# Optimization experiments

Hardware: AMD Instinct MI355X
Metric: run time of the kernel (lower is better)

Reference implementation:

```python
import jax, jax.numpy as jnp
import numpy as np

EPS = 1e-5

def _round_ste(x):
    # straight-through round (identical value in fwd; STE grad in bwd module)
    return x + jax.lax.stop_gradient(jnp.round(x) - x)

def _quant_weight(w, bits):
    # per-tensor symmetric absmax quantization to `bits` bits (BitNet-style)
    qb = float(2 ** (bits - 1) - 1)
    scale = qb / jnp.maximum(jnp.max(jnp.abs(w)), EPS)
    return _round_ste(jnp.clip(w * scale, -qb, qb)) / scale

def _quant_act(x):
    # per-token 8-bit absmax activation quantization
    qb = 127.0
    scale = qb / jnp.maximum(jnp.max(jnp.abs(x), axis=-1, keepdims=True), EPS)
    return _round_ste(jnp.clip(x * scale, -qb, qb)) / scale

def _layernorm(x, gamma, beta):
    mu = jnp.mean(x, axis=-1, keepdims=True)
    var = jnp.mean(jnp.square(x - mu), axis=-1, keepdims=True)
    return (x - mu) * jax.lax.rsqrt(var + EPS) * gamma + beta

def _qlinear(x, w, b, bits):
    return jnp.einsum('btd,fd->btf', _quant_act(x), _quant_weight(w, bits)) + b

def setup_inputs() -> dict:
    key = jax.random.key(0)
    ks = jax.random.split(key, 4)
    B, T, D, F = 8, 2048, 1024, 4096
    return {
        'x': jax.random.normal(ks[0], (B, T, D), dtype=jnp.float32),
        'mask': jnp.ones((B, T, 1), dtype=jnp.float32),
        'ln_gamma': jnp.ones((D,), dtype=jnp.float32),
        'ln_beta': jnp.zeros((D,), dtype=jnp.float32),
        'w1': jax.random.normal(ks[1], (F, D), dtype=jnp.float32) * (1.0 / np.sqrt(D)),
        'b1': jnp.zeros((F,), dtype=jnp.float32),
        'w2': jax.random.normal(ks[2], (D, F), dtype=jnp.float32) * (1.0 / np.sqrt(F)),
        'b2': jnp.zeros((D,), dtype=jnp.float32),
        'bitwidth': 8,
    }

def reference(x, mask, ln_gamma, ln_beta, w1, b1, w2, b2, bitwidth):
    y = _layernorm(x, ln_gamma, ln_beta)           # [B,T,D]
    y = _qlinear(y, w1, b1, bitwidth)              # [B,T,F]
    y = y * jax.nn.sigmoid(y)                      # swish
    y = _qlinear(y, w2, b2, bitwidth)              # [B,T,D]
    seq_mask = mask[:, :, 0][..., None]            # [B,T,1]
    y = y * seq_mask
    return x + 0.5 * y
```

## Files before the change

kernel.cpp:

```cpp
#include <hip/hip_runtime.h>
#include <hip/hip_bf16.h>
#include <stdint.h>


typedef int v4i __attribute__((ext_vector_type(4)));
typedef int v16i __attribute__((ext_vector_type(16)));

#define BK 128

__device__ __forceinline__ float wave_max64(float v) {
#pragma unroll
  for (int off = 32; off; off >>= 1) v = fmaxf(v, __shfl_xor(v, off, 64));
  return v;
}

__device__ __forceinline__ void load16_to_lds(const int8_t* g, int8_t* l) {
  __builtin_amdgcn_global_load_lds((const __attribute__((address_space(1))) void*)g,
                                   (__attribute__((address_space(3))) void*)l, 16, 0, 0);
}

__global__ __launch_bounds__(256) void absmax_kernel(const float* __restrict__ w, int n4,
                                                     int* __restrict__ slot) {
  float m = 0.f;
  const float4* w4 = (const float4*)w;
  for (int i = blockIdx.x * 256 + threadIdx.x; i < n4; i += gridDim.x * 256) {
    float4 v = w4[i];
    m = fmaxf(fmaxf(fabsf(v.x), fabsf(v.y)), fmaxf(fmaxf(fabsf(v.z), fabsf(v.w)), m));
  }
  m = wave_max64(m);
  __shared__ float sm[4];
  int lane = threadIdx.x & 63, wv = threadIdx.x >> 6;
  if (!lane) sm[wv] = m;
  __syncthreads();
  if (!threadIdx.x) {
    m = fmaxf(fmaxf(sm[0], sm[1]), fmaxf(sm[2], sm[3]));
    atomicMax(slot, __float_as_int(m));
  }
}

__global__ void scales_kernel(const int* __restrict__ wmax, const int* __restrict__ bits,
                              float* __restrict__ scal) {
  float qb = (float)((1 << (bits[0] - 1)) - 1);
  scal[2] = qb / fmaxf(__int_as_float(wmax[0]), 1e-5f);
  scal[3] = qb / fmaxf(__int_as_float(wmax[1]), 1e-5f);
  scal[4] = qb;
}

__global__ __launch_bounds__(256) void wquant_kernel(const float* __restrict__ w,
                                                     const float* __restrict__ scal, int which,
                                                     int8_t* __restrict__ out) {
  float s = scal[2 + which], qb = scal[4];
  int i = blockIdx.x * 256 + threadIdx.x;
  float4 v = ((const float4*)w)[i];
  char4 q;
  q.x = (char)(int)rintf(fminf(fmaxf(v.x * s, -qb), qb));
  q.y = (char)(int)rintf(fminf(fmaxf(v.y * s, -qb), qb));
  q.z = (char)(int)rintf(fminf(fmaxf(v.z * s, -qb), qb));
  q.w = (char)(int)rintf(fminf(fmaxf(v.w * s, -qb), qb));
  ((char4*)out)[i] = q;
}

__global__ __launch_bounds__(256) void ln_quant_kernel(const float* __restrict__ x,
                                                       const float* __restrict__ gamma,
                                                       const float* __restrict__ beta,
                                                       int8_t* __restrict__ xq,
                                                       float* __restrict__ xscale) {
  const int row = blockIdx.x;
  const int tid = threadIdx.x;
  const float4 v = ((const float4*)(x + (size_t)row * 1024))[tid];
  float s = v.x + v.y + v.z + v.w;
  float ss = fmaf(v.x, v.x, fmaf(v.y, v.y, fmaf(v.z, v.z, v.w * v.w)));
#pragma unroll
  for (int off = 32; off; off >>= 1) {
    s += __shfl_xor(s, off, 64);
    ss += __shfl_xor(ss, off, 64);
  }
  __shared__ float sm[8];
  const int lane = tid & 63, wv = tid >> 6;
  if (!lane) { sm[wv] = s; sm[4 + wv] = ss; }
  __syncthreads();
  s = sm[0] + sm[1] + sm[2] + sm[3];
  ss = sm[4] + sm[5] + sm[6] + sm[7];
  const float mu = s * (1.f / 1024.f);
  const float var = ss * (1.f / 1024.f) - mu * mu;
  const float rstd = rsqrtf(var + 1e-5f);
  const float4 g = ((const float4*)gamma)[tid];
  const float4 bb = ((const float4*)beta)[tid];
  float y0 = (v.x - mu) * rstd * g.x + bb.x;
  float y1 = (v.y - mu) * rstd * g.y + bb.y;
  float y2 = (v.z - mu) * rstd * g.z + bb.z;
  float y3 = (v.w - mu) * rstd * g.w + bb.w;
  float am = fmaxf(fmaxf(fabsf(y0), fabsf(y1)), fmaxf(fabsf(y2), fabsf(y3)));
  am = wave_max64(am);
  __syncthreads();
  if (!lane) sm[wv] = am;
  __syncthreads();
  am = fmaxf(fmaxf(sm[0], sm[1]), fmaxf(sm[2], sm[3]));
  const float scale = 127.f / fmaxf(am, 1e-5f);
  char4 q;
  q.x = (char)(int)rintf(fminf(fmaxf(y0 * scale, -127.f), 127.f));
  q.y = (char)(int)rintf(fminf(fmaxf(y1 * scale, -127.f), 127.f));
  q.z = (char)(int)rintf(fminf(fmaxf(y2 * scale, -127.f), 127.f));
  q.w = (char)(int)rintf(fminf(fmaxf(y3 * scale, -127.f), 127.f));
  ((char4*)(xq + (size_t)row * 1024))[tid] = q;
  if (!tid) xscale[row] = scale;
}

__global__ __launch_bounds__(256) void hquant_kernel(const ushort* __restrict__ h,
                                                     int8_t* __restrict__ hq,
                                                     float* __restrict__ hscale) {
  const int row = blockIdx.x;
  const int tid = threadIdx.x;
  const int4* p = (const int4*)(h + (size_t)row * 4096);
  union { int4 i4; ushort u[8]; } ua, ub;
  ua.i4 = p[tid * 2];
  ub.i4 = p[tid * 2 + 1];
  float f[16];
#pragma unroll
  for (int i = 0; i < 8; ++i) f[i] = __uint_as_float((unsigned)ua.u[i] << 16);
#pragma unroll
  for (int i = 0; i < 8; ++i) f[8 + i] = __uint_as_float((unsigned)ub.u[i] << 16);
  float am = 0.f;
#pragma unroll
  for (int i = 0; i < 16; ++i) am = fmaxf(am, fabsf(f[i]));
  am = wave_max64(am);
  __shared__ float sm[4];
  const int lane = tid & 63, wv = tid >> 6;
  if (!lane) sm[wv] = am;
  __syncthreads();
  am = fmaxf(fmaxf(sm[0], sm[1]), fmaxf(sm[2], sm[3]));
  const float scale = 127.f / fmaxf(am, 1e-5f);
  union { int4 i4; char c[16]; } q;
#pragma unroll
  for (int i = 0; i < 16; ++i)
    q.c[i] = (char)(int)rintf(fminf(fmaxf(f[i] * scale, -127.f), 127.f));
  ((int4*)(hq + (size_t)row * 4096))[tid] = q.i4;
  if (!tid) hscale[row] = scale;
}

template <int K, int BMt, int BNt>
__device__ __forceinline__ void gemm_core(const int8_t* __restrict__ A,
                                          const int8_t* __restrict__ B, int8_t* As, int8_t* Bs,
                                          v16i (&acc)[BMt / 64][BNt / 64]) {
  constexpr int AM = BMt / 64, AN = BNt / 64;
  const int tid = threadIdx.x;
  const int lane = tid & 63;
  const int wave = tid >> 6;
  const int wm = (wave & 1) * (BMt / 2);
  const int wn = (wave >> 1) * (BNt / 2);
  const int lrow = lane & 31;
  const int half = lane >> 5;
  const int x7 = lrow & 7;
  const size_t m0 = (size_t)blockIdx.y * BMt;
  const size_t n0 = (size_t)blockIdx.x * BNt;

  const int r = tid >> 3;
  const int cs = ((tid & 7) ^ (r & 7)) << 4;
  const int8_t* ga = A + (m0 + r) * K + cs;
  const int8_t* gb = B + (n0 + r) * K + cs;
  int8_t* la = As + tid * 16;
  int8_t* lb = Bs + tid * 16;

  for (int k0 = 0; k0 < K; k0 += BK) {
    __syncthreads();
#pragma unroll
    for (int t = 0; t < BMt / 32; ++t)
      load16_to_lds(ga + (size_t)(t * 32) * K + k0, la + t * 4096);
#pragma unroll
    for (int t = 0; t < BNt / 32; ++t)
      load16_to_lds(gb + (size_t)(t * 32) * K + k0, lb + t * 4096);
    __syncthreads();
#pragma unroll
    for (int ks = 0; ks < 4; ++ks) {
      const int so = ((ks * 2 + half) ^ x7) << 4;
      v4i af[AM], bf[AN];
#pragma unroll
      for (int i = 0; i < AM; ++i)
        af[i] = *(const v4i*)(As + (wm + i * 32 + lrow) * 128 + so);
#pragma unroll
      for (int j = 0; j < AN; ++j)
        bf[j] = *(const v4i*)(Bs + (wn + j * 32 + lrow) * 128 + so);
#pragma unroll
      for (int i = 0; i < AM; ++i)
#pragma unroll
        for (int j = 0; j < AN; ++j)
          acc[i][j] = __builtin_amdgcn_mfma_i32_32x32x32_i8(af[i], bf[j], acc[i][j], 0, 0, 0);
    }
  }
}

__global__ __launch_bounds__(256, 2) void gemm1_kernel(const int8_t* __restrict__ Aq,
                                                       const int8_t* __restrict__ Bq,
                                                       const float* __restrict__ xscale,
                                                       const float* __restrict__ scal,
                                                       const float* __restrict__ bias,
                                                       ushort* __restrict__ H) {
  __shared__ __align__(16) int8_t As[128 * 128];
  __shared__ __align__(16) int8_t Bs[256 * 128];
  v16i acc[2][4] = {};
  gemm_core<1024, 128, 256>(Aq, Bq, As, Bs, acc);
  const float sw1 = scal[2];
  const int lane = threadIdx.x & 63;
  const int wave = threadIdx.x >> 6;
  const int m0 = blockIdx.y * 128 + (wave & 1) * 64;
  const int n0 = blockIdx.x * 256 + (wave >> 1) * 128;
  const int cn = lane & 31;
  const int h4 = (lane >> 5) << 2;
#pragma unroll
  for (int i = 0; i < 2; ++i) {
#pragma unroll
    for (int reg = 0; reg < 16; ++reg) {
      const int row = (reg & 3) + ((reg >> 2) << 3) + h4;
      const int m = m0 + i * 32 + row;
      const float rcp = 1.0f / (xscale[m] * sw1);
#pragma unroll
      for (int j = 0; j < 4; ++j) {
        const int n = n0 + j * 32 + cn;
        const float v = (float)acc[i][j][reg] * rcp + bias[n];
        const float hsw = v / (1.0f + __expf(-v));
        __hip_bfloat16 hb = __float2bfloat16(hsw);
        H[(size_t)m * 4096 + n] = *(const ushort*)&hb;
      }
    }
  }
}

__global__ __launch_bounds__(256, 2) void gemm2_kernel(const int8_t* __restrict__ Aq,
                                                       const int8_t* __restrict__ Bq,
                                                       const float* __restrict__ hscale,
                                                       const float* __restrict__ scal,
                                                       const float* __restrict__ bias,
                                                       const float* __restrict__ x,
                                                       const float* __restrict__ mask,
                                                       float* __restrict__ out) {
  __shared__ __align__(16) int8_t As[256 * 128];
  __shared__ __align__(16) int8_t Bs[128 * 128];
  v16i acc[4][2] = {};
  gemm_core<4096, 256, 128>(Aq, Bq, As, Bs, acc);
  const float sw2 = scal[3];
  const int lane = threadIdx.x & 63;
  const int wave = threadIdx.x >> 6;
  const int m0 = blockIdx.y * 256 + (wave & 1) * 128;
  const int n0 = blockIdx.x * 128 + (wave >> 1) * 64;
  const int cn = lane & 31;
  const int h4 = (lane >> 5) << 2;
#pragma unroll
  for (int i = 0; i < 4; ++i) {
#pragma unroll
    for (int reg = 0; reg < 16; ++reg) {
      const int row = (reg & 3) + ((reg >> 2) << 3) + h4;
      const int m = m0 + i * 32 + row;
      const float rcp = 1.0f / (hscale[m] * sw2);
      const float mk = 0.5f * mask[m];
#pragma unroll
      for (int j = 0; j < 2; ++j) {
        const int n = n0 + j * 32 + cn;
        const float v = (float)acc[i][j][reg] * rcp + bias[n];
        const size_t idx = (size_t)m * 1024 + n;
        out[idx] = x[idx] + mk * v;
      }
    }
  }
}

extern "C" void kernel_launch(void* const* d_in, const int* in_sizes, int n_in, void* d_out,
                              int out_size, void* d_ws, size_t ws_size, hipStream_t stream) {
  const float* x = (const float*)d_in[0];
  const float* mask = (const float*)d_in[1];
  const float* gamma = (const float*)d_in[2];
  const float* beta = (const float*)d_in[3];
  const float* w1 = (const float*)d_in[4];
  const float* b1 = (const float*)d_in[5];
  const float* w2 = (const float*)d_in[6];
  const float* b2 = (const float*)d_in[7];
  const int* bits = (const int*)d_in[8];
  float* out = (float*)d_out;

  char* ws = (char*)d_ws;
  int* wmax = (int*)ws;
  float* scal = (float*)ws;
  float* xscale = (float*)(ws + (1u << 20));
  float* hscale = (float*)(ws + (2u << 20));
  int8_t* w1q = (int8_t*)(ws + (4u << 20));
  int8_t* w2q = (int8_t*)(ws + (8u << 20));
  int8_t* xq = (int8_t*)(ws + (12u << 20));
  int8_t* hq = (int8_t*)(ws + (28u << 20));
  ushort* h = (ushort*)(ws + (size_t)(92u << 20));

  const int NW = 4096 * 1024;

  absmax_kernel<<<1024, 256, 0, stream>>>(w1, NW / 4, wmax + 0);
  absmax_kernel<<<1024, 256, 0, stream>>>(w2, NW / 4, wmax + 1);
  scales_kernel<<<1, 1, 0, stream>>>(wmax, bits, scal);
  wquant_kernel<<<NW / 1024, 256, 0, stream>>>(w1, scal, 0, w1q);
  wquant_kernel<<<NW / 1024, 256, 0, stream>>>(w2, scal, 1, w2q);
  ln_quant_kernel<<<16384, 256, 0, stream>>>(x, gamma, beta, xq, xscale);
  gemm1_kernel<<<dim3(4096 / 256, 16384 / 128), 256, 0, stream>>>(xq, w1q, xscale, scal, b1, h);
  hquant_kernel<<<16384, 256, 0, stream>>>(h, hq, hscale);
  gemm2_kernel<<<dim3(1024 / 128, 16384 / 256), 256, 0, stream>>>(hq, w2q, hscale, scal, b2, x,
                                                                  mask, out);
}
```

Baseline: 421.4 us.

## Double-buffer int8 GEMM tiles with 256x256 blocks and XCD-aware block remap

Replaces the single-buffered GEMM core with a version that uses 256x256 output tiles per 512-thread block and two LDS buffers. The next K-slice is prefetched with global_load_lds while MFMAs run on the current slice, and wave priority is raised around the MFMA burst. Blocks are launched on a 1D grid and remapped so consecutive blocks on the same XCD share M rows, which should improve L2 reuse. The cost is 128KB of LDS per block, which limits occupancy to one block per CU, and gemm2 now launches only 256 blocks.

Result: slower. 484.7 us (+15.0%).

```diff
diff --git a/kernel.cpp b/kernel.cpp
--- a/kernel.cpp
+++ b/kernel.cpp
@@ -5,8 +5,6 @@
 
 typedef int v4i __attribute__((ext_vector_type(4)));
 typedef int v16i __attribute__((ext_vector_type(16)));
-
-#define BK 128
 
 __device__ __forceinline__ float wave_max64(float v) {
 #pragma unroll
@@ -138,21 +136,20 @@
   if (!tid) hscale[row] = scale;
 }
 
-template <int K, int BMt, int BNt>
-__device__ __forceinline__ void gemm_core(const int8_t* __restrict__ A,
-                                          const int8_t* __restrict__ B, int8_t* As, int8_t* Bs,
-                                          v16i (&acc)[BMt / 64][BNt / 64]) {
-  constexpr int AM = BMt / 64, AN = BNt / 64;
+template <int K>
+__device__ __forceinline__ void gemm_core8(const int8_t* __restrict__ A,
+                                           const int8_t* __restrict__ B, int8_t* As, int8_t* Bs,
+                                           v16i (&acc)[4][2], int mIdx, int nIdx) {
   const int tid = threadIdx.x;
   const int lane = tid & 63;
   const int wave = tid >> 6;
-  const int wm = (wave & 1) * (BMt / 2);
-  const int wn = (wave >> 1) * (BNt / 2);
+  const int wm = (wave & 1) * 128;
+  const int wn = (wave >> 1) * 64;
   const int lrow = lane & 31;
   const int half = lane >> 5;
   const int x7 = lrow & 7;
-  const size_t m0 = (size_t)blockIdx.y * BMt;
-  const size_t n0 = (size_t)blockIdx.x * BNt;
+  const size_t m0 = (size_t)mIdx * 256;
+  const size_t n0 = (size_t)nIdx * 256;
 
   const int r = tid >> 3;
   const int cs = ((tid & 7) ^ (r & 7)) << 4;
@@ -161,60 +158,86 @@
   int8_t* la = As + tid * 16;
   int8_t* lb = Bs + tid * 16;
 
-  for (int k0 = 0; k0 < K; k0 += BK) {
-    __syncthreads();
-#pragma unroll
-    for (int t = 0; t < BMt / 32; ++t)
-      load16_to_lds(ga + (size_t)(t * 32) * K + k0, la + t * 4096);
-#pragma unroll
-    for (int t = 0; t < BNt / 32; ++t)
-      load16_to_lds(gb + (size_t)(t * 32) * K + k0, lb + t * 4096);
-    __syncthreads();
-#pragma unroll
-    for (int ks = 0; ks < 4; ++ks) {
-      const int so = ((ks * 2 + half) ^ x7) << 4;
-      v4i af[AM], bf[AN];
-#pragma unroll
-      for (int i = 0; i < AM; ++i)
-        af[i] = *(const v4i*)(As + (wm + i * 32 + lrow) * 128 + so);
-#pragma unroll
-      for (int j = 0; j < AN; ++j)
-        bf[j] = *(const v4i*)(Bs + (wn + j * 32 + lrow) * 128 + so);
-#pragma unroll
-      for (int i = 0; i < AM; ++i)
-#pragma unroll
-        for (int j = 0; j < AN; ++j)
+  constexpr int NT = K / 128;
+
+#pragma unroll
+  for (int p = 0; p < 4; ++p) {
+    load16_to_lds(ga + (size_t)(p * 64) * K, la + p * 8192);
+    load16_to_lds(gb + (size_t)(p * 64) * K, lb + p * 8192);
+  }
+  asm volatile("s_waitcnt vmcnt(0)" ::: "memory");
+  __builtin_amdgcn_sched_barrier(0);
+  __builtin_amdgcn_s_barrier();
+
+  for (int kt = 0; kt < NT; ++kt) {
+    const int buf = kt & 1;
+    const int8_t* Ab = As + buf * 32768;
+    const int8_t* Bb = Bs + buf * 32768;
+    int8_t* lan = la + (buf ^ 1) * 32768;
+    int8_t* lbn = lb + (buf ^ 1) * 32768;
+    const size_t knext = (size_t)(kt + 1) * 128;
+    const bool pf = (kt + 1 < NT);
+#pragma unroll
+    for (int p = 0; p < 4; ++p) {
+      if (pf) {
+        load16_to_lds(ga + (size_t)(p * 64) * K + knext, lan + p * 8192);
+        load16_to_lds(gb + (size_t)(p * 64) * K + knext, lbn + p * 8192);
+      }
+      const int so = ((p * 2 + half) ^ x7) << 4;
+      v4i af[4], bf[2];
+#pragma unroll
+      for (int i = 0; i < 4; ++i)
+        af[i] = *(const v4i*)(Ab + (wm + i * 32 + lrow) * 128 + so);
+#pragma unroll
+      for (int j = 0; j < 2; ++j)
+        bf[j] = *(const v4i*)(Bb + (wn + j * 32 + lrow) * 128 + so);
+      __builtin_amdgcn_s_barrier();
+      __builtin_amdgcn_s_setprio(1);
+#pragma unroll
+      for (int i = 0; i < 4; ++i)
+#pragma unroll
+        for (int j = 0; j < 2; ++j)
           acc[i][j] = __builtin_amdgcn_mfma_i32_32x32x32_i8(af[i], bf[j], acc[i][j], 0, 0, 0);
+      __builtin_amdgcn_s_setprio(0);
+      if (p == 3) {
+        if (pf) asm volatile("s_waitcnt vmcnt(0)" ::: "memory");
+        __builtin_amdgcn_sched_barrier(0);
+      }
+      __builtin_amdgcn_s_barrier();
     }
   }
 }
 
-__global__ __launch_bounds__(256, 2) void gemm1_kernel(const int8_t* __restrict__ Aq,
+__global__ __launch_bounds__(512, 2) void gemm1_kernel(const int8_t* __restrict__ Aq,
                                                        const int8_t* __restrict__ Bq,
                                                        const float* __restrict__ xscale,
                                                        const float* __restrict__ scal,
                                                        const float* __restrict__ bias,
                                                        ushort* __restrict__ H) {
-  __shared__ __align__(16) int8_t As[128 * 128];
-  __shared__ __align__(16) int8_t Bs[256 * 128];
-  v16i acc[2][4] = {};
-  gemm_core<1024, 128, 256>(Aq, Bq, As, Bs, acc);
+  __shared__ __align__(16) int8_t As[2 * 256 * 128];
+  __shared__ __align__(16) int8_t Bs[2 * 256 * 128];
+  const int bid = blockIdx.x;
+  const int logical = (bid & 7) * 128 + (bid >> 3);
+  const int mIdx = logical >> 4;
+  const int nIdx = logical & 15;
+  v16i acc[4][2] = {};
+  gemm_core8<1024>(Aq, Bq, As, Bs, acc, mIdx, nIdx);
   const float sw1 = scal[2];
   const int lane = threadIdx.x & 63;
   const int wave = threadIdx.x >> 6;
-  const int m0 = blockIdx.y * 128 + (wave & 1) * 64;
-  const int n0 = blockIdx.x * 256 + (wave >> 1) * 128;
+  const int m0 = mIdx * 256 + (wave & 1) * 128;
+  const int n0 = nIdx * 256 + (wave >> 1) * 64;
   const int cn = lane & 31;
   const int h4 = (lane >> 5) << 2;
 #pragma unroll
-  for (int i = 0; i < 2; ++i) {
+  for (int i = 0; i < 4; ++i) {
 #pragma unroll
     for (int reg = 0; reg < 16; ++reg) {
       const int row = (reg & 3) + ((reg >> 2) << 3) + h4;
       const int m = m0 + i * 32 + row;
       const float rcp = 1.0f / (xscale[m] * sw1);
 #pragma unroll
-      for (int j = 0; j < 4; ++j) {
+      for (int j = 0; j < 2; ++j) {
         const int n = n0 + j * 32 + cn;
         const float v = (float)acc[i][j][reg] * rcp + bias[n];
         const float hsw = v / (1.0f + __expf(-v));
@@ -225,7 +248,7 @@
   }
 }
 
-__global__ __launch_bounds__(256, 2) void gemm2_kernel(const int8_t* __restrict__ Aq,
+__global__ __launch_bounds__(512, 2) void gemm2_kernel(const int8_t* __restrict__ Aq,
                                                        const int8_t* __restrict__ Bq,
                                                        const float* __restrict__ hscale,
                                                        const float* __restrict__ scal,
@@ -233,15 +256,19 @@
                                                        const float* __restrict__ x,
                                                        const float* __restrict__ mask,
                                                        float* __restrict__ out) {
-  __shared__ __align__(16) int8_t As[256 * 128];
-  __shared__ __align__(16) int8_t Bs[128 * 128];
+  __shared__ __align__(16) int8_t As[2 * 256 * 128];
+  __shared__ __align__(16) int8_t Bs[2 * 256 * 128];
+  const int bid = blockIdx.x;
+  const int logical = (bid & 7) * 32 + (bid >> 3);
+  const int mIdx = logical >> 2;
+  const int nIdx = logical & 3;
   v16i acc[4][2] = {};
-  gemm_core<4096, 256, 128>(Aq, Bq, As, Bs, acc);
+  gemm_core8<4096>(Aq, Bq, As, Bs, acc, mIdx, nIdx);
   const float sw2 = scal[3];
   const int lane = threadIdx.x & 63;
   const int wave = threadIdx.x >> 6;
-  const int m0 = blockIdx.y * 256 + (wave & 1) * 128;
-  const int n0 = blockIdx.x * 128 + (wave >> 1) * 64;
+  const int m0 = mIdx * 256 + (wave & 1) * 128;
+  const int n0 = nIdx * 256 + (wave >> 1) * 64;
   const int cn = lane & 31;
   const int h4 = (lane >> 5) << 2;
 #pragma unroll
@@ -295,8 +322,7 @@
   wquant_kernel<<<NW / 1024, 256, 0, stream>>>(w1, scal, 0, w1q);
   wquant_kernel<<<NW / 1024, 256, 0, stream>>>(w2, scal, 1, w2q);
   ln_quant_kernel<<<16384, 256, 0, stream>>>(x, gamma, beta, xq, xscale);
-  gemm1_kernel<<<dim3(4096 / 256, 16384 / 128), 256, 0, stream>>>(xq, w1q, xscale, scal, b1, h);
+  gemm1_kernel<<<1024, 512, 0, stream>>>(xq, w1q, xscale, scal, b1, h);
   hquant_kernel<<<16384, 256, 0, stream>>>(h, hq, hscale);
-  gemm2_kernel<<<dim3(1024 / 128, 16384 / 256), 256, 0, stream>>>(hq, w2q, hscale, scal, b2, x,
-                                                                  mask, out);
-}
+  gemm2_kernel<<<256, 512, 0, stream>>>(hq, w2q, hscale, scal, b2, x, mask, out);
+}
```
